# Kernel tuning notes

Hardware: AMD Instinct MI355X
Metric: run time of the kernel (lower is better)

Reference implementation:

```python
import jax, jax.numpy as jnp
import numpy as np

INPUT, HIDDEN, OUTPUT = 512, 512, 512
B, S = 32, 2048


def setup_inputs() -> dict:
    key = jax.random.key(0)
    ks = jax.random.split(key, 8)
    s_in = 1.0 / np.sqrt(INPUT)
    s_h = 1.0 / np.sqrt(HIDDEN)
    return {
        "x": jax.random.normal(ks[0], (B, S, INPUT), dtype=jnp.float32),
        "W_xh": jax.random.uniform(ks[1], (HIDDEN, INPUT), jnp.float32, -s_in, s_in),
        "b_xh": jax.random.uniform(ks[2], (HIDDEN,), jnp.float32, -s_in, s_in),
        "W_hh": jax.random.uniform(ks[3], (HIDDEN, HIDDEN), jnp.float32, -s_h, s_h),
        "b_hh": jax.random.uniform(ks[4], (HIDDEN,), jnp.float32, -s_h, s_h),
        "b_h": jnp.zeros((HIDDEN,), jnp.float32),
        "W_fc": jax.random.uniform(ks[5], (OUTPUT, HIDDEN), jnp.float32, -s_h, s_h),
        "b_fc": jax.random.uniform(ks[6], (OUTPUT,), jnp.float32, -s_h, s_h),
    }


def reference(x, W_xh, b_xh, W_hh, b_hh, b_h, W_fc, b_fc):
    # Precompute the input projection for all timesteps in one big GEMM:
    # [B,S,I] @ [I,H] -> [B,S,H]; bias terms folded in once.
    xproj = jnp.einsum("bsi,hi->bsh", x, W_xh) + (b_xh + b_hh + b_h)
    h0 = jnp.zeros((x.shape[0], W_hh.shape[0]), x.dtype)

    def step(h, xp_t):
        h = jnp.tanh(xp_t + h @ W_hh.T)
        return h, None

    # scan over time: xproj transposed to [S,B,H]
    h_final, _ = jax.lax.scan(step, h0, jnp.swapaxes(xproj, 0, 1))
    return h_final @ W_fc.T + b_fc
```

## Files before the change

kernel.cpp:

```cpp
#include <hip/hip_runtime.h>

typedef _Float16 f16;
typedef _Float16 f16x8 __attribute__((ext_vector_type(8)));
typedef float    f32x4 __attribute__((ext_vector_type(4)));

#define NSTEP 2048
#define HID   512
#define BATCH 32
#define SEQL  2048

#define P1_AS 40

__global__ __launch_bounds__(256, 2) void xproj_kernel(
    const float* __restrict__ x, const float* __restrict__ Wxh,
    const float* __restrict__ bxh, const float* __restrict__ bhh,
    const float* __restrict__ bh, f16* __restrict__ xp)
{
    __shared__ __align__(16) f16 As[64 * P1_AS];
    __shared__ __align__(16) f16 Bs[512 * P1_AS];

    const int t = threadIdx.x;
    const int wave = t >> 6, lane = t & 63;
    const size_t mbase = (size_t)blockIdx.x * 64;

    f32x4 acc[4][8];
#pragma unroll
    for (int i = 0; i < 4; i++)
#pragma unroll
        for (int j = 0; j < 8; j++) acc[i][j] = (f32x4){0.f, 0.f, 0.f, 0.f};

    const int r_st = t >> 2;
    const int koff = (t & 3) * 8;

    for (int k0 = 0; k0 < 512; k0 += 32) {
        __syncthreads();
        {
            const float* src = x + (mbase + r_st) * 512 + k0 + koff;
            float4 a0 = *(const float4*)src;
            float4 a1 = *(const float4*)(src + 4);
            f16x8 h;
            h[0] = (f16)a0.x; h[1] = (f16)a0.y; h[2] = (f16)a0.z; h[3] = (f16)a0.w;
            h[4] = (f16)a1.x; h[5] = (f16)a1.y; h[6] = (f16)a1.z; h[7] = (f16)a1.w;
            *(f16x8*)&As[r_st * P1_AS + koff] = h;
        }
#pragma unroll
        for (int i = 0; i < 8; i++) {
            int n = r_st + i * 64;
            const float* src = Wxh + (size_t)n * 512 + k0 + koff;
            float4 b0 = *(const float4*)src;
            float4 b1 = *(const float4*)(src + 4);
            f16x8 h;
            h[0] = (f16)b0.x; h[1] = (f16)b0.y; h[2] = (f16)b0.z; h[3] = (f16)b0.w;
            h[4] = (f16)b1.x; h[5] = (f16)b1.y; h[6] = (f16)b1.z; h[7] = (f16)b1.w;
            *(f16x8*)&Bs[n * P1_AS + koff] = h;
        }
        __syncthreads();

        f16x8 af[4];
#pragma unroll
        for (int rt = 0; rt < 4; rt++)
            af[rt] = *(const f16x8*)&As[(rt * 16 + (lane & 15)) * P1_AS + (lane >> 4) * 8];
#pragma unroll
        for (int ct = 0; ct < 8; ct++) {
            f16x8 bf = *(const f16x8*)&Bs[((wave * 8 + ct) * 16 + (lane & 15)) * P1_AS + (lane >> 4) * 8];
#pragma unroll
            for (int rt = 0; rt < 4; rt++)
                acc[rt][ct] = __builtin_amdgcn_mfma_f32_16x16x32_f16(af[rt], bf, acc[rt][ct], 0, 0, 0);
        }
    }

#pragma unroll
    for (int ct = 0; ct < 8; ct++) {
        int n = wave * 128 + ct * 16 + (lane & 15);
        float bias = bxh[n] + bhh[n] + bh[n];
#pragma unroll
        for (int rt = 0; rt < 4; rt++) {
#pragma unroll
            for (int r = 0; r < 4; r++) {
                size_t m = mbase + rt * 16 + (lane >> 4) * 4 + r;
                xp[m * 512 + n] = (f16)(acc[rt][ct][r] + bias);
            }
        }
    }
}

#define P2_LDS_BYTES (2 * HID * 2 + 8 * 16 * 64 * 16)

__global__ __launch_bounds__(512, 1) void rnn_kernel(
    const float* __restrict__ Whh, const f16* __restrict__ xp,
    f16* __restrict__ hfin)
{
    extern __shared__ __align__(16) char smem[];
    f16* hbuf0 = (f16*)smem;
    f16* hbuf1 = hbuf0 + HID;
    f16* ldsB  = hbuf1 + HID;

    const int t = threadIdx.x;
    const int wave = t >> 6, lane = t & 63;
    const int b = blockIdx.x;

    const int c_in = lane & 15;
    const int k8   = (lane >> 4) * 8;

    f16x8 wreg[48];
#pragma unroll
    for (int r = 0; r < 3; r++) {
        const float* wrow = Whh + (size_t)((wave * 4 + r) * 16 + c_in) * 512;
#pragma unroll
        for (int kf = 0; kf < 16; kf++) {
            float4 w0 = *(const float4*)(wrow + kf * 32 + k8);
            float4 w1 = *(const float4*)(wrow + kf * 32 + k8 + 4);
            f16x8 h;
            h[0] = (f16)w0.x; h[1] = (f16)w0.y; h[2] = (f16)w0.z; h[3] = (f16)w0.w;
            h[4] = (f16)w1.x; h[5] = (f16)w1.y; h[6] = (f16)w1.z; h[7] = (f16)w1.w;
            wreg[r * 16 + kf] = h;
        }
    }
    {
        const float* wrow = Whh + (size_t)((wave * 4 + 3) * 16 + c_in) * 512;
#pragma unroll
        for (int kf = 0; kf < 16; kf++) {
            float4 w0 = *(const float4*)(wrow + kf * 32 + k8);
            float4 w1 = *(const float4*)(wrow + kf * 32 + k8 + 4);
            f16x8 h;
            h[0] = (f16)w0.x; h[1] = (f16)w0.y; h[2] = (f16)w0.z; h[3] = (f16)w0.w;
            h[4] = (f16)w1.x; h[5] = (f16)w1.y; h[6] = (f16)w1.z; h[7] = (f16)w1.w;
            *(f16x8*)&ldsB[(size_t)wave * 8192 + kf * 512 + lane * 8] = h;
        }
    }
    hbuf0[t & (HID - 1)] = (f16)0.f;
    __syncthreads();

    const f16* xprow = xp + (size_t)b * SEQL * 512 + wave * 64 + lane;
    const int ldsb_base = wave * 8192 + lane * 8;

    float xv = (float)xprow[0];
    for (int s = 0; s < NSTEP; s++) {
        const f16* cur = (s & 1) ? hbuf1 : hbuf0;
        f16*       nxt = (s & 1) ? hbuf0 : hbuf1;
        int sn = (s + 1 < NSTEP) ? s + 1 : s;
        float xv_next = (float)xprow[(size_t)sn * 512];

        f32x4 a0 = (f32x4){0.f,0.f,0.f,0.f}, a1 = a0, a2 = a0, a3 = a0;
#pragma unroll
        for (int kf = 0; kf < 16; kf++) {
            f16x8 av = *(const f16x8*)&cur[kf * 32 + k8];
            a0 = __builtin_amdgcn_mfma_f32_16x16x32_f16(av, wreg[kf],      a0, 0, 0, 0);
            a1 = __builtin_amdgcn_mfma_f32_16x16x32_f16(av, wreg[16 + kf], a1, 0, 0, 0);
            a2 = __builtin_amdgcn_mfma_f32_16x16x32_f16(av, wreg[32 + kf], a2, 0, 0, 0);
            f16x8 bl = *(const f16x8*)&ldsB[ldsb_base + kf * 512];
            a3 = __builtin_amdgcn_mfma_f32_16x16x32_f16(av, bl, a3, 0, 0, 0);
        }
        int r = lane >> 4;
        float v = (r == 0) ? a0[0] : (r == 1) ? a1[0] : (r == 2) ? a2[0] : a3[0];
        v += xv;
        float e = __expf(2.f * v);
        v = 1.f - 2.f / (e + 1.f);
        nxt[wave * 64 + lane] = (f16)v;
        xv = xv_next;
        __syncthreads();
    }
    hfin[(size_t)b * 512 + t] = hbuf0[t & (HID - 1)];
}

#define P3_HS 520

__global__ __launch_bounds__(256, 2) void fc_kernel(
    const f16* __restrict__ hfin, const float* __restrict__ Wfc,
    const float* __restrict__ bfc, float* __restrict__ out)
{
    __shared__ __align__(16) f16 hs[BATCH * P3_HS];
    const int t = threadIdx.x;
    for (int i = 0; i < 64; i++) {
        int e = i * 256 + t;
        hs[(e >> 9) * P3_HS + (e & 511)] = hfin[e];
    }
    __syncthreads();

    const int bidx = t & 31;
    const int oi = t >> 5;
    const int o0 = blockIdx.x * 16;
    const int oA = o0 + oi, oB = o0 + oi + 8;
    const float* wA = Wfc + (size_t)oA * 512;
    const float* wB = Wfc + (size_t)oB * 512;

    float sA = 0.f, sB = 0.f;
#pragma unroll 4
    for (int kb = 0; kb < 64; kb++) {
        f16x8 hv = *(const f16x8*)&hs[bidx * P3_HS + kb * 8];
        float4 wa0 = *(const float4*)(wA + kb * 8);
        float4 wa1 = *(const float4*)(wA + kb * 8 + 4);
        float4 wb0 = *(const float4*)(wB + kb * 8);
        float4 wb1 = *(const float4*)(wB + kb * 8 + 4);
        float h0 = (float)hv[0], h1 = (float)hv[1], h2 = (float)hv[2], h3 = (float)hv[3];
        float h4 = (float)hv[4], h5 = (float)hv[5], h6 = (float)hv[6], h7 = (float)hv[7];
        sA += wa0.x*h0 + wa0.y*h1 + wa0.z*h2 + wa0.w*h3 + wa1.x*h4 + wa1.y*h5 + wa1.z*h6 + wa1.w*h7;
        sB += wb0.x*h0 + wb0.y*h1 + wb0.z*h2 + wb0.w*h3 + wb1.x*h4 + wb1.y*h5 + wb1.z*h6 + wb1.w*h7;
    }
    out[(size_t)bidx * 512 + oA] = sA + bfc[oA];
    out[(size_t)bidx * 512 + oB] = sB + bfc[oB];
}

extern "C" void kernel_launch(void* const* d_in, const int* in_sizes, int n_in,
                              void* d_out, int out_size, void* d_ws, size_t ws_size,
                              hipStream_t stream) {
    const float* x    = (const float*)d_in[0];
    const float* Wxh  = (const float*)d_in[1];
    const float* bxh  = (const float*)d_in[2];
    const float* Whh  = (const float*)d_in[3];
    const float* bhh  = (const float*)d_in[4];
    const float* bh   = (const float*)d_in[5];
    const float* Wfc  = (const float*)d_in[6];
    const float* bfc  = (const float*)d_in[7];
    float* outp = (float*)d_out;

    f16* xp   = (f16*)d_ws;
    f16* hfin = (f16*)((char*)d_ws + (size_t)BATCH * SEQL * 512 * 2);

    hipFuncSetAttribute((const void*)rnn_kernel,
                        hipFuncAttributeMaxDynamicSharedMemorySize, 160 * 1024);

    xproj_kernel<<<(BATCH * SEQL) / 64, 256, 0, stream>>>(x, Wxh, bxh, bhh, bh, xp);
    rnn_kernel<<<BATCH, 512, P2_LDS_BYTES, stream>>>(Whh, xp, hfin);
    fc_kernel<<<32, 256, 0, stream>>>(hfin, Wfc, bfc, outp);
}
```

Before: 2.801 ms.

## Replace MFMA recurrence with per-thread fdot2 row dot products and global h buffer

The recurrent kernel now gives each thread one full row of W_hh. It keeps 416 fp16 weights in registers as packed half2 and the last 96 in LDS, and computes its hidden unit with v_dot2 instructions instead of 16x16 MFMA tiles. The hidden state is double-buffered in a global workspace, read as uniform float4 loads (a zero-offset asm trick keeps them as vector loads), and each step ends with a block barrier. This removes the MFMA work that was wasted on batch-1 tiles and the lane select, at the cost of very high register pressure, serialized dot-product latency per thread, and global-memory round trips for h each step.

```diff
diff --git a/kernel.cpp b/kernel.cpp
--- a/kernel.cpp
+++ b/kernel.cpp
@@ -1,6 +1,7 @@
 #include <hip/hip_runtime.h>
 
 typedef _Float16 f16;
+typedef _Float16 f16x2 __attribute__((ext_vector_type(2)));
 typedef _Float16 f16x8 __attribute__((ext_vector_type(8)));
 typedef float    f32x4 __attribute__((ext_vector_type(4)));
 
@@ -84,83 +85,102 @@
     }
 }
 
-#define P2_LDS_BYTES (2 * HID * 2 + 8 * 16 * 64 * 16)
-
-__global__ __launch_bounds__(512, 1) void rnn_kernel(
+#define REGP   208
+#define TAILP  48
+#define TSTR   52
+#define P2_LDS_BYTES (HID * TSTR * 4)
+
+__global__ __launch_bounds__(512) void rnn_kernel(
     const float* __restrict__ Whh, const f16* __restrict__ xp,
-    f16* __restrict__ hfin)
+    f16* __restrict__ hx, f16* __restrict__ hfin)
 {
     extern __shared__ __align__(16) char smem[];
-    f16* hbuf0 = (f16*)smem;
-    f16* hbuf1 = hbuf0 + HID;
-    f16* ldsB  = hbuf1 + HID;
+    f16x2* tail = (f16x2*)smem;
 
     const int t = threadIdx.x;
-    const int wave = t >> 6, lane = t & 63;
     const int b = blockIdx.x;
-
-    const int c_in = lane & 15;
-    const int k8   = (lane >> 4) * 8;
-
-    f16x8 wreg[48];
-#pragma unroll
-    for (int r = 0; r < 3; r++) {
-        const float* wrow = Whh + (size_t)((wave * 4 + r) * 16 + c_in) * 512;
-#pragma unroll
-        for (int kf = 0; kf < 16; kf++) {
-            float4 w0 = *(const float4*)(wrow + kf * 32 + k8);
-            float4 w1 = *(const float4*)(wrow + kf * 32 + k8 + 4);
-            f16x8 h;
-            h[0] = (f16)w0.x; h[1] = (f16)w0.y; h[2] = (f16)w0.z; h[3] = (f16)w0.w;
-            h[4] = (f16)w1.x; h[5] = (f16)w1.y; h[6] = (f16)w1.z; h[7] = (f16)w1.w;
-            wreg[r * 16 + kf] = h;
-        }
-    }
-    {
-        const float* wrow = Whh + (size_t)((wave * 4 + 3) * 16 + c_in) * 512;
-#pragma unroll
-        for (int kf = 0; kf < 16; kf++) {
-            float4 w0 = *(const float4*)(wrow + kf * 32 + k8);
-            float4 w1 = *(const float4*)(wrow + kf * 32 + k8 + 4);
-            f16x8 h;
-            h[0] = (f16)w0.x; h[1] = (f16)w0.y; h[2] = (f16)w0.z; h[3] = (f16)w0.w;
-            h[4] = (f16)w1.x; h[5] = (f16)w1.y; h[6] = (f16)w1.z; h[7] = (f16)w1.w;
-            *(f16x8*)&ldsB[(size_t)wave * 8192 + kf * 512 + lane * 8] = h;
-        }
-    }
-    hbuf0[t & (HID - 1)] = (f16)0.f;
+    const int n = t;
+
+    const float4* wrow4 = (const float4*)(Whh + (size_t)n * 512);
+    f16x2 wreg[REGP];
+#pragma unroll
+    for (int j4 = 0; j4 < REGP / 2; j4++) {
+        float4 w = wrow4[j4];
+        f16x2 p0; p0[0] = (f16)w.x; p0[1] = (f16)w.y;
+        f16x2 p1; p1[0] = (f16)w.z; p1[1] = (f16)w.w;
+        wreg[2 * j4]     = p0;
+        wreg[2 * j4 + 1] = p1;
+    }
+#pragma unroll
+    for (int j4 = 0; j4 < TAILP / 2; j4++) {
+        float4 w = wrow4[REGP / 2 + j4];
+        f16x2 p0; p0[0] = (f16)w.x; p0[1] = (f16)w.y;
+        f16x2 p1; p1[0] = (f16)w.z; p1[1] = (f16)w.w;
+        tail[n * TSTR + 2 * j4]     = p0;
+        tail[n * TSTR + 2 * j4 + 1] = p1;
+    }
     __syncthreads();
 
-    const f16* xprow = xp + (size_t)b * SEQL * 512 + wave * 64 + lane;
-    const int ldsb_base = wave * 8192 + lane * 8;
+    int zoff;
+    asm volatile("v_mov_b32 %0, 0" : "=v"(zoff));
+
+    const f16* xprow = xp + (size_t)b * SEQL * 512 + n;
+    f16* hx0 = hx + (size_t)b * 2 * HID;
 
     float xv = (float)xprow[0];
+    f16 hn = (f16)0.f;
+
     for (int s = 0; s < NSTEP; s++) {
-        const f16* cur = (s & 1) ? hbuf1 : hbuf0;
-        f16*       nxt = (s & 1) ? hbuf0 : hbuf1;
         int sn = (s + 1 < NSTEP) ? s + 1 : s;
         float xv_next = (float)xprow[(size_t)sn * 512];
 
-        f32x4 a0 = (f32x4){0.f,0.f,0.f,0.f}, a1 = a0, a2 = a0, a3 = a0;
-#pragma unroll
-        for (int kf = 0; kf < 16; kf++) {
-            f16x8 av = *(const f16x8*)&cur[kf * 32 + k8];
-            a0 = __builtin_amdgcn_mfma_f32_16x16x32_f16(av, wreg[kf],      a0, 0, 0, 0);
-            a1 = __builtin_amdgcn_mfma_f32_16x16x32_f16(av, wreg[16 + kf], a1, 0, 0, 0);
-            a2 = __builtin_amdgcn_mfma_f32_16x16x32_f16(av, wreg[32 + kf], a2, 0, 0, 0);
-            f16x8 bl = *(const f16x8*)&ldsB[ldsb_base + kf * 512];
-            a3 = __builtin_amdgcn_mfma_f32_16x16x32_f16(av, bl, a3, 0, 0, 0);
-        }
-        int r = lane >> 4;
-        float v = (r == 0) ? a0[0] : (r == 1) ? a1[0] : (r == 2) ? a2[0] : a3[0];
-        v += xv;
+        float v;
+        if (s > 0) {
+            const float4* hp = (const float4*)((const char*)(hx0 + (s & 1) * HID) + zoff);
+            float a0 = 0.f, a1 = 0.f, a2 = 0.f, a3 = 0.f;
+#pragma unroll
+            for (int j = 0; j < REGP / 4; j++) {
+                float4 hv = hp[j];
+                f16x2 p0 = ((const f16x2*)&hv)[0];
+                f16x2 p1 = ((const f16x2*)&hv)[1];
+                f16x2 p2 = ((const f16x2*)&hv)[2];
+                f16x2 p3 = ((const f16x2*)&hv)[3];
+                a0 = __builtin_amdgcn_fdot2(wreg[4 * j + 0], p0, a0, false);
+                a1 = __builtin_amdgcn_fdot2(wreg[4 * j + 1], p1, a1, false);
+                a2 = __builtin_amdgcn_fdot2(wreg[4 * j + 2], p2, a2, false);
+                a3 = __builtin_amdgcn_fdot2(wreg[4 * j + 3], p3, a3, false);
+            }
+#pragma unroll
+            for (int j2 = 0; j2 < TAILP / 4; j2++) {
+                float4 hv = hp[REGP / 4 + j2];
+                f16x8 tv = *(const f16x8*)&tail[n * TSTR + 4 * j2];
+                f16x2 q0 = ((const f16x2*)&tv)[0];
+                f16x2 q1 = ((const f16x2*)&tv)[1];
+                f16x2 q2 = ((const f16x2*)&tv)[2];
+                f16x2 q3 = ((const f16x2*)&tv)[3];
+                f16x2 p0 = ((const f16x2*)&hv)[0];
+                f16x2 p1 = ((const f16x2*)&hv)[1];
+                f16x2 p2 = ((const f16x2*)&hv)[2];
+                f16x2 p3 = ((const f16x2*)&hv)[3];
+                a0 = __builtin_amdgcn_fdot2(q0, p0, a0, false);
+                a1 = __builtin_amdgcn_fdot2(q1, p1, a1, false);
+                a2 = __builtin_amdgcn_fdot2(q2, p2, a2, false);
+                a3 = __builtin_amdgcn_fdot2(q3, p3, a3, false);
+            }
+            v = (a0 + a1) + (a2 + a3) + xv;
+        } else {
+            v = xv;
+        }
         float e = __expf(2.f * v);
         v = 1.f - 2.f / (e + 1.f);
-        nxt[wave * 64 + lane] = (f16)v;
+        hn = (f16)v;
+
+        hx0[((s + 1) & 1) * HID + n] = hn;
         xv = xv_next;
         __syncthreads();
     }
-    hfin[(size_t)b * 512 + t] = hbuf0[t & (HID - 1)];
+
+    hfin[(size_t)b * 512 + n] = hn;
 }
 
 #define P3_HS 520
@@ -214,13 +234,15 @@
     const float* bfc  = (const float*)d_in[7];
     float* outp = (float*)d_out;
 
-    f16* xp   = (f16*)d_ws;
-    f16* hfin = (f16*)((char*)d_ws + (size_t)BATCH * SEQL * 512 * 2);
+    char* ws = (char*)d_ws;
+    f16* xp   = (f16*)ws;
+    f16* hfin = (f16*)(ws + (size_t)BATCH * SEQL * 512 * 2);
+    f16* hx   = (f16*)(ws + (size_t)BATCH * SEQL * 512 * 2 + 32768);
 
     hipFuncSetAttribute((const void*)rnn_kernel,
                         hipFuncAttributeMaxDynamicSharedMemorySize, 160 * 1024);
 
     xproj_kernel<<<(BATCH * SEQL) / 64, 256, 0, stream>>>(x, Wxh, bxh, bhh, bh, xp);
-    rnn_kernel<<<BATCH, 512, P2_LDS_BYTES, stream>>>(Whh, xp, hfin);
+    rnn_kernel<<<BATCH, 512, P2_LDS_BYTES, stream>>>(Whh, xp, hx, hfin);
     fc_kernel<<<32, 256, 0, stream>>>(hfin, Wfc, bfc, outp);
 }
```

Result: slower. 8.370 ms (+198.8%).
